# Performance work log

Hardware: AMD Instinct MI355X
Metric: run time of the kernel (lower is better)

Reference implementation:

```python
import jax, jax.numpy as jnp
import numpy as np

B, S, H = 2, 2048, 2048
NUM_HEADS, HEAD_DIM, GROUP_SIZE = 16, 128, 4
NUM_KV_HEADS = NUM_HEADS // GROUP_SIZE
ROPE_THETA = 10000.0


def setup_inputs() -> dict:
    key = jax.random.key(0)
    ks = jax.random.split(key, 10)
    xavier = lambda k, fi, fo: jax.random.uniform(k, (fi, fo), jnp.float32,
                                                  -jnp.sqrt(6.0 / (fi + fo)), jnp.sqrt(6.0 / (fi + fo)))
    hidden_states = jax.random.normal(ks[0], (B, S, H), jnp.float32)
    # causal mask: 1.0 where attention is disallowed (strictly upper triangle)
    mask = jnp.triu(jnp.ones((S, S), jnp.float32), k=1)[None, None, :, :]
    mask = jnp.broadcast_to(mask, (B, 1, S, S))
    return {
        "hidden_states": hidden_states,
        "mask": mask,
        "Wq": xavier(ks[1], H, NUM_HEADS * HEAD_DIM), "bq": jnp.zeros((NUM_HEADS * HEAD_DIM,), jnp.float32),
        "Wk": xavier(ks[2], H, NUM_KV_HEADS * HEAD_DIM), "bk": jnp.zeros((NUM_KV_HEADS * HEAD_DIM,), jnp.float32),
        "Wv": xavier(ks[3], H, NUM_KV_HEADS * HEAD_DIM), "bv": jnp.zeros((NUM_KV_HEADS * HEAD_DIM,), jnp.float32),
        "Wo": xavier(ks[4], NUM_HEADS * HEAD_DIM, H), "bo": jnp.zeros((H,), jnp.float32),
    }


def _apply_rope(q, k):
    # q: [b, s, hq, d], k: [b, s, hk, d]
    s, d = q.shape[1], q.shape[-1]
    inv_freq = 1.0 / (ROPE_THETA ** (jnp.arange(0, d, 2, dtype=jnp.float32) / d))  # [d/2]
    angles = jnp.arange(s, dtype=jnp.float32)[:, None] * inv_freq[None, :]          # [s, d/2]
    cos = jnp.cos(angles)[None, :, None, :]  # [1, s, 1, d/2]
    sin = jnp.sin(angles)[None, :, None, :]

    def rot(x):
        x1, x2 = jnp.split(x, 2, axis=-1)
        return jnp.concatenate([x1 * cos - x2 * sin, x1 * sin + x2 * cos], axis=-1)

    return rot(q), rot(k)


def reference(hidden_states, mask, Wq, bq, Wk, bk, Wv, bv, Wo, bo):
    b, s, _ = hidden_states.shape
    scale = 1.0 / jnp.sqrt(jnp.float32(HEAD_DIM))

    q = (hidden_states @ Wq + bq).reshape(b, s, NUM_HEADS, HEAD_DIM)
    k = (hidden_states @ Wk + bk).reshape(b, s, NUM_KV_HEADS, HEAD_DIM)
    v = (hidden_states @ Wv + bv).reshape(b, s, NUM_KV_HEADS, HEAD_DIM)

    q, k = _apply_rope(q, k)

    q = jnp.transpose(q, (0, 2, 1, 3))  # [b, hq, s, d]
    k = jnp.transpose(k, (0, 2, 1, 3))  # [b, hk, s, d]
    v = jnp.transpose(v, (0, 2, 1, 3))

    new_past_key, new_past_value = k, v

    # GQA: repeat each KV head group_size times
    k_rep = jnp.repeat(k, GROUP_SIZE, axis=1)  # [b, hq, s, d]
    v_rep = jnp.repeat(v, GROUP_SIZE, axis=1)

    attn_scores = jnp.einsum('bhqd,bhkd->bhqk', q, k_rep) * scale  # [b, hq, s, s]
    attn_scores = attn_scores + mask * -1e9
    attn_probs = jax.nn.softmax(attn_scores, axis=-1)
    attn_output = jnp.einsum('bhqk,bhkd->bhqd', attn_probs, v_rep)

    attn_output = attn_output.transpose(0, 2, 1, 3).reshape(b, s, NUM_HEADS * HEAD_DIM)
    attn_output = attn_output @ Wo + bo
    return attn_output, new_past_key, new_past_value
```

## Files before the change

### kernel.cpp

```cpp
#include <hip/hip_runtime.h>
#include <stdint.h>

#define S_LEN 2048
#define HDIM  2048
#define N_HEADS 16
#define HEAD_D 128
#define N_KV 4

typedef unsigned short u16;
typedef __attribute__((ext_vector_type(8))) short bf16x8;
typedef __attribute__((ext_vector_type(4))) short bf16x4;
typedef __attribute__((ext_vector_type(4))) float f32x4;

#define MFMA_PV(a, b, c) __builtin_amdgcn_mfma_f32_16x16x16bf16_1k(a, b, c, 0, 0, 0)

__device__ __forceinline__ u16 f2bf(float f) {
  unsigned u = __float_as_uint(f);
  u += 0x7FFFu + ((u >> 16) & 1u);
  return (u16)(u >> 16);
}

__device__ __forceinline__ float bf2f(u16 v) {
  return __uint_as_float(((unsigned)v) << 16);
}

__device__ __forceinline__ void gll16(void* lds, const void* gp) {
  __builtin_amdgcn_global_load_lds(
      (const __attribute__((address_space(1))) void*)gp,
      (__attribute__((address_space(3))) void*)lds, 16, 0, 0);
}

__device__ __forceinline__ void wtrans_body(
    const float* __restrict__ W, u16* __restrict__ Wt, int K, int N,
    int perm, int flat, float (*tile)[65]) {
  int k0 = (flat & 31) * 64, n0 = (flat >> 5) * 64;
  int tr = threadIdx.x >> 6, tc = threadIdx.x & 63;
#pragma unroll
  for (int i = 0; i < 16; ++i) {
    int r = tr + i * 4;
    tile[r][tc] = W[(size_t)(k0 + r) * N + n0 + tc];
  }
  __syncthreads();
#pragma unroll
  for (int i = 0; i < 16; ++i) {
    int r = tr + i * 4;
    int nn = n0 + r;
    if (perm)
      nn = (nn & ~127) | ((nn & 15) | ((nn & 48) << 1) | ((nn & 64) >> 2));
    Wt[(size_t)nn * K + k0 + tc] = f2bf(tile[tc][r]);
  }
}

__global__ __launch_bounds__(256) void k_prep(
    const float* __restrict__ hs, u16* __restrict__ Xbf,
    const float* __restrict__ Wq, u16* __restrict__ Wqt,
    const float* __restrict__ Wk, u16* __restrict__ Wkt,
    const float* __restrict__ Wv, u16* __restrict__ Wvt,
    const float* __restrict__ Wo, u16* __restrict__ Wot,
    float2* __restrict__ trig) {
  __shared__ float tile[64][65];
  const int bid = blockIdx.x;
  if (bid < 8192) {
    int i = bid * 256 + threadIdx.x;
    float4 v = ((const float4*)hs)[i];
    ushort4 o;
    o.x = f2bf(v.x); o.y = f2bf(v.y); o.z = f2bf(v.z); o.w = f2bf(v.w);
    ((ushort4*)Xbf)[i] = o;
  } else if (bid < 9216) {
    wtrans_body(Wq, Wqt, 2048, 2048, 1, bid - 8192, tile);
  } else if (bid < 9472) {
    wtrans_body(Wk, Wkt, 2048, 512, 1, bid - 9216, tile);
  } else if (bid < 9728) {
    wtrans_body(Wv, Wvt, 2048, 512, 0, bid - 9472, tile);
  } else if (bid < 10752) {
    wtrans_body(Wo, Wot, 2048, 2048, 0, bid - 9728, tile);
  } else {
    const float c1 = -13.287712379549449f / 64.f;
    int idx = (bid - 10752) * 256 + threadIdx.x;
    int s = idx >> 6, d1 = idx & 63;
    float fr = exp2f((float)d1 * c1);
    float sn, cs;
    sincosf((float)s * fr, &sn, &cs);
    trig[idx] = make_float2(cs, sn);
  }
}

__device__ __forceinline__ void gemm_main_128(
    const u16* __restrict__ A, const u16* __restrict__ Bt,
    int m0, int n0, int K, f32x4 (&acc)[4][4]) {
  __shared__ __align__(16) u16 sA[128 * 32];
  __shared__ __align__(16) u16 sB[128 * 32];
  const int tid = threadIdx.x;
  const int lane = tid & 63;
  const int wave = tid >> 6;
  const int quad = lane >> 4;
  const int l15 = lane & 15;
  const int wm = (wave >> 1) << 6;
  const int wn = (wave & 1) << 6;

#pragma unroll
  for (int i = 0; i < 4; ++i)
#pragma unroll
    for (int j = 0; j < 4; ++j)
      acc[i][j] = (f32x4){0.f, 0.f, 0.f, 0.f};

  for (int kk = 0; kk < K; kk += 32) {
    __syncthreads();
#pragma unroll
    for (int it = 0; it < 2; ++it) {
      int c = tid + (it << 8);
      int row = c >> 2;
      int ko = (c & 3) << 3;
      gll16((char*)sA + c * 16, A + (size_t)(m0 + row) * K + kk + ko);
      gll16((char*)sB + c * 16, Bt + (size_t)(n0 + row) * K + kk + ko);
    }
    __syncthreads();
    bf16x8 af[4], bfr[4];
#pragma unroll
    for (int i = 0; i < 4; ++i)
      af[i] = *(const bf16x8*)&sA[(wm + (i << 4) + l15) * 32 + quad * 8];
#pragma unroll
    for (int j = 0; j < 4; ++j)
      bfr[j] = *(const bf16x8*)&sB[(wn + (j << 4) + l15) * 32 + quad * 8];
#pragma unroll
    for (int i = 0; i < 4; ++i)
#pragma unroll
      for (int j = 0; j < 4; ++j)
        acc[i][j] = __builtin_amdgcn_mfma_f32_16x16x32_bf16(af[i], bfr[j], acc[i][j], 0, 0, 0);
  }
}

__device__ __forceinline__ void gemm_tile_128(
    const u16* __restrict__ A, const u16* __restrict__ Bt,
    const float* __restrict__ bias, float* __restrict__ C,
    int m0, int n0, int K, int ldc) {
  const int tid = threadIdx.x;
  const int lane = tid & 63;
  const int wave = tid >> 6;
  const int quad = lane >> 4;
  const int l15 = lane & 15;
  const int wm = (wave >> 1) << 6;
  const int wn = (wave & 1) << 6;

  f32x4 acc[4][4];
  gemm_main_128(A, Bt, m0, n0, K, acc);

#pragma unroll
  for (int i = 0; i < 4; ++i) {
    int row = m0 + wm + (i << 4) + quad * 4;
#pragma unroll
    for (int j = 0; j < 4; ++j) {
      int col = n0 + wn + (j << 4) + l15;
      float bv = bias[col];
      float* cp = C + (size_t)row * ldc + col;
#pragma unroll
      for (int r = 0; r < 4; ++r)
        cp[(size_t)r * ldc] = acc[i][j][r] + bv;
    }
  }
}

__global__ __launch_bounds__(256) void k_gemm_qkv_fused(
    const u16* __restrict__ X, const u16* __restrict__ Wqt,
    const u16* __restrict__ Wkt, const u16* __restrict__ Wvt,
    const float* __restrict__ bq, const float* __restrict__ bk,
    const float* __restrict__ bv, u16* __restrict__ Qbf,
    u16* __restrict__ Kbf, float* __restrict__ outK,
    u16* __restrict__ Vt, float* __restrict__ outV,
    const float2* __restrict__ trig) {
  const int m0 = blockIdx.x << 7;
  const int by = blockIdx.y;
  const int tid = threadIdx.x;
  const int lane = tid & 63;
  const int wave = tid >> 6;
  const int quad = lane >> 4;
  const int l15 = lane & 15;
  const int wm = (wave >> 1) << 6;
  const int wn = (wave & 1) << 6;

  const u16* Bt; int n0;
  if (by < 16)      { Bt = Wqt; n0 = by << 7; }
  else if (by < 20) { Bt = Wkt; n0 = (by - 16) << 7; }
  else              { Bt = Wvt; n0 = (by - 20) << 7; }

  f32x4 acc[4][4];
  gemm_main_128(X, Bt, m0, n0, 2048, acc);

  if (by < 16) {
    const float qscale = 0.08838834764831845f * 1.4426950408889634f;
    const int h = by;
#pragma unroll
    for (int jp = 0; jp < 2; ++jp) {
      const int d1 = (((wn >> 5) + jp) << 4) + l15;
      const float b1 = bq[h * 128 + d1];
      const float b2 = bq[h * 128 + d1 + 64];
#pragma unroll
      for (int i = 0; i < 4; ++i) {
        const int rowb = m0 + wm + (i << 4) + quad * 4;
#pragma unroll
        for (int r = 0; r < 4; ++r) {
          const int tok = rowb + r;
          const int b = tok >> 11, s = tok & 2047;
          const float2 t = trig[(s << 6) + d1];
          float x1 = acc[i][2 * jp][r] + b1;
          float x2 = acc[i][2 * jp + 1][r] + b2;
          u16* dst = Qbf + ((size_t)(b * N_HEADS + h) * S_LEN + s) * HEAD_D + d1;
          dst[0]  = f2bf((x1 * t.x - x2 * t.y) * qscale);
          dst[64] = f2bf((x1 * t.y + x2 * t.x) * qscale);
        }
      }
    }
  } else if (by < 20) {
    const int kvh = by - 16;
#pragma unroll
    for (int jp = 0; jp < 2; ++jp) {
      const int d1 = (((wn >> 5) + jp) << 4) + l15;
      const float b1 = bk[kvh * 128 + d1];
      const float b2 = bk[kvh * 128 + d1 + 64];
#pragma unroll
      for (int i = 0; i < 4; ++i) {
        const int rowb = m0 + wm + (i << 4) + quad * 4;
#pragma unroll
        for (int r = 0; r < 4; ++r) {
          const int tok = rowb + r;
          const int b = tok >> 11, s = tok & 2047;
          const float2 t = trig[(s << 6) + d1];
          float x1 = acc[i][2 * jp][r] + b1;
          float x2 = acc[i][2 * jp + 1][r] + b2;
          float o1 = x1 * t.x - x2 * t.y;
          float o2 = x1 * t.y + x2 * t.x;
          size_t idx = ((size_t)(b * N_KV + kvh) * S_LEN + s) * HEAD_D + d1;
          Kbf[idx]      = f2bf(o1);
          Kbf[idx + 64] = f2bf(o2);
          outK[idx]      = o1;
          outK[idx + 64] = o2;
        }
      }
    }
  } else {
    const int kvh = by - 20;
#pragma unroll
    for (int i = 0; i < 4; ++i) {
      const int rowb = m0 + wm + (i << 4) + quad * 4;
      const int b = rowb >> 11, s = rowb & 2047;
      const int z = b * N_KV + kvh;
#pragma unroll
      for (int j = 0; j < 4; ++j) {
        const int d = wn + (j << 4) + l15;
        const float bvv = bv[kvh * 128 + d];
        float v0 = acc[i][j][0] + bvv;
        float v1 = acc[i][j][1] + bvv;
        float v2 = acc[i][j][2] + bvv;
        float v3 = acc[i][j][3] + bvv;
        float* ov = outV + ((size_t)z * S_LEN + s) * HEAD_D + d;
        ov[0]   = v0;
        ov[128] = v1;
        ov[256] = v2;
        ov[384] = v3;
        ushort4 pk;
        pk.x = f2bf(v0); pk.y = f2bf(v1); pk.z = f2bf(v2); pk.w = f2bf(v3);
        *(ushort4*)(Vt + ((size_t)z * HEAD_D + d) * S_LEN + s) = pk;
      }
    }
  }
}

__global__ __launch_bounds__(256) void k_gemm_o(
    const u16* __restrict__ A, const u16* __restrict__ Wot,
    const float* __restrict__ bo, float* __restrict__ C) {
  gemm_tile_128(A, Wot, bo, C, blockIdx.x << 7, blockIdx.y << 7, 2048, 2048);
}

__global__ __launch_bounds__(256, 2) void k_attn(
    const u16* __restrict__ Qbf, const u16* __restrict__ Kbf,
    const u16* __restrict__ Vt, u16* __restrict__ attn,
    u16* __restrict__ pO, float* __restrict__ pML) {
  __shared__ __align__(16) u16 smem[17920];
  u16* sK = smem;
  u16* sV = smem + 8704;

  const int tid = threadIdx.x;
  const int lane = tid & 63;
  const int wave = tid >> 6;
  const int quad = lane >> 4;
  const int l15 = lane & 15;

  const int by = blockIdx.y;
  int qt, t0, t1, slot;
  bool finalw;
  if (by < 8) {
    qt = 8 + by; t0 = 0; t1 = 16; finalw = false;
    slot = ((blockIdx.x << 3) + (qt - 8)) << 1;
  } else {
    qt = 23 - by;
    if (qt >= 8) {
      t0 = 16; t1 = 2 * qt + 2; finalw = false;
      slot = (((blockIdx.x << 3) + (qt - 8)) << 1) + 1;
    } else {
      t0 = 0; t1 = 2 * qt + 2; finalw = true; slot = 0;
    }
  }

  const int bh = blockIdx.x;
  const int b = bh >> 4;
  const int h = bh & 15;
  const int kvh = h >> 2;
  const int q0 = qt << 7;
  const int qw = q0 + wave * 32;

  const u16* Qb = Qbf + ((size_t)(b * N_HEADS + h) * S_LEN + qw) * HEAD_D;
  const u16* Kb = Kbf + (size_t)(b * N_KV + kvh) * S_LEN * HEAD_D;
  const u16* Vb = Vt + (size_t)(b * N_KV + kvh) * HEAD_D * S_LEN;

  bf16x8 aq[2][4];
#pragma unroll
  for (int i = 0; i < 2; ++i)
#pragma unroll
    for (int kc = 0; kc < 4; ++kc)
      aq[i][kc] = *(const bf16x8*)(Qb + (size_t)(i * 16 + l15) * HEAD_D + kc * 32 + quad * 8);

  float mst[2] = {-1e30f, -1e30f}, lst[2] = {0.f, 0.f};
  f32x4 oacc[2][8];
#pragma unroll
  for (int i = 0; i < 2; ++i)
#pragma unroll
    for (int n = 0; n < 8; ++n) oacc[i][n] = (f32x4){0.f, 0.f, 0.f, 0.f};

  for (int t = t0; t < t1; ++t) {
    const int kt0 = t << 6;
    __syncthreads();
#pragma unroll
    for (int it = 0; it < 9; ++it) {
      int c = tid + (it << 8);
      if (c < 1088) {
        int row = c / 17;
        int k16 = c - row * 17;
        gll16((char*)sK + c * 16, Kb + (size_t)(kt0 + row) * HEAD_D + k16 * 8);
      } else if (c < 2240) {
        int vv = c - 1088;
        int d = vv / 9;
        int s16 = vv - d * 9;
        gll16((char*)sV + vv * 16, Vb + (size_t)d * S_LEN + kt0 + s16 * 8);
      }
    }
    __syncthreads();

    if (kt0 > qw + 31) continue;

    f32x4 st[2][4];
#pragma unroll
    for (int i = 0; i < 2; ++i)
#pragma unroll
      for (int j = 0; j < 4; ++j) st[i][j] = (f32x4){0.f, 0.f, 0.f, 0.f};
#pragma unroll
    for (int kc = 0; kc < 4; ++kc) {
#pragma unroll
      for (int j = 0; j < 4; ++j) {
        bf16x8 kf = *(const bf16x8*)&sK[(j * 16 + l15) * 136 + kc * 32 + quad * 8];
#pragma unroll
        for (int i = 0; i < 2; ++i)
          st[i][j] = __builtin_amdgcn_mfma_f32_16x16x32_bf16(kf, aq[i][kc], st[i][j], 0, 0, 0);
      }
    }

    if (kt0 + 63 > qw) {
#pragma unroll
      for (int i = 0; i < 2; ++i) {
        int q = qw + i * 16 + l15;
#pragma unroll
        for (int j = 0; j < 4; ++j) {
          int s = kt0 + j * 16 + quad * 4;
#pragma unroll
          for (int r = 0; r < 4; ++r)
            if (s + r > q) st[i][j][r] = -1e9f;
        }
      }
    }

    bf16x4 pf[2][4];
    float al[2];
#pragma unroll
    for (int i = 0; i < 2; ++i) {
      float m = -1e30f;
#pragma unroll
      for (int j = 0; j < 4; ++j)
#pragma unroll
        for (int r = 0; r < 4; ++r) m = fmaxf(m, st[i][j][r]);
      m = fmaxf(m, __shfl_xor(m, 16, 64));
      m = fmaxf(m, __shfl_xor(m, 32, 64));
      float mn = fmaxf(mst[i], m);
      al[i] = exp2f(mst[i] - mn);
      mst[i] = mn;
      float rs = 0.f;
#pragma unroll
      for (int j = 0; j < 4; ++j) {
        float p0 = exp2f(st[i][j][0] - mn);
        float p1 = exp2f(st[i][j][1] - mn);
        float p2 = exp2f(st[i][j][2] - mn);
        float p3 = exp2f(st[i][j][3] - mn);
        rs += (p0 + p1) + (p2 + p3);
        union { unsigned u[2]; bf16x4 v; } pk;
        pk.u[0] = __builtin_amdgcn_perm(__float_as_uint(p1) + 0x8000u,
                                        __float_as_uint(p0) + 0x8000u, 0x07060302u);
        pk.u[1] = __builtin_amdgcn_perm(__float_as_uint(p3) + 0x8000u,
                                        __float_as_uint(p2) + 0x8000u, 0x07060302u);
        pf[i][j] = pk.v;
      }
      rs += __shfl_xor(rs, 16, 64);
      rs += __shfl_xor(rs, 32, 64);
      lst[i] = lst[i] * al[i] + rs;
#pragma unroll
      for (int r = 0; r < 4; ++r) {
        float a = __shfl(al[i], quad * 4 + r, 16);
#pragma unroll
        for (int n = 0; n < 8; ++n) oacc[i][n][r] *= a;
      }
    }

#pragma unroll
    for (int j = 0; j < 4; ++j) {
#pragma unroll
      for (int n = 0; n < 8; ++n) {
        bf16x4 vf = *(const bf16x4*)&sV[(n * 16 + l15) * 72 + j * 16 + quad * 4];
#pragma unroll
        for (int i = 0; i < 2; ++i)
          oacc[i][n] = MFMA_PV(pf[i][j], vf, oacc[i][n]);
      }
    }
  }

  if (finalw) {
#pragma unroll
    for (int i = 0; i < 2; ++i)
#pragma unroll
      for (int r = 0; r < 4; ++r) {
        float inv = 1.0f / __shfl(lst[i], quad * 4 + r, 16);
        int row = qw + i * 16 + quad * 4 + r;
        u16* op = attn + ((size_t)b * S_LEN + row) * HDIM + h * HEAD_D;
#pragma unroll
        for (int n = 0; n < 8; ++n)
          op[n * 16 + l15] = f2bf(oacc[i][n][r] * inv);
      }
  } else {
    u16* po = pO + (size_t)slot * 16384;
#pragma unroll
    for (int i = 0; i < 2; ++i)
#pragma unroll
      for (int r = 0; r < 4; ++r) {
        int row = wave * 32 + i * 16 + quad * 4 + r;
#pragma unroll
        for (int n = 0; n < 8; ++n)
          po[row * 128 + n * 16 + l15] = f2bf(oacc[i][n][r]);
      }
    if (quad == 0) {
      float* ml = pML + slot * 256;
#pragma unroll
      for (int i = 0; i < 2; ++i) {
        int row = wave * 32 + i * 16 + l15;
        ml[row] = mst[i];
        ml[128 + row] = lst[i];
      }
    }
  }
}

__global__ __launch_bounds__(256) void k_attn_combine(
    const u16* __restrict__ pO, const float* __restrict__ pML,
    u16* __restrict__ attn) {
  const int bh = blockIdx.x;
  const int qt = 8 + blockIdx.y;
  const int b = bh >> 4;
  const int h = bh & 15;
  const int s0 = ((bh << 3) + blockIdx.y) << 1;
  const int row = threadIdx.x >> 1;
  const int half = threadIdx.x & 1;

  const float* ml0 = pML + s0 * 256;
  const float* ml1 = pML + (s0 + 1) * 256;
  float m0 = ml0[row], l0 = ml0[128 + row];
  float m1 = ml1[row], l1 = ml1[128 + row];
  float m = fmaxf(m0, m1);
  float w0 = exp2f(m0 - m), w1 = exp2f(m1 - m);
  float inv = 1.0f / (l0 * w0 + l1 * w1);
  w0 *= inv; w1 *= inv;

  const u16* o0 = pO + (size_t)s0 * 16384 + row * 128 + half * 64;
  const u16* o1 = o0 + 16384;
  u16* op = attn + ((size_t)(b * S_LEN + (qt << 7) + row)) * HDIM + h * HEAD_D + half * 64;
#pragma unroll
  for (int k = 0; k < 8; ++k) {
    ushort4 a0 = ((const ushort4*)o0)[k * 2];
    ushort4 b0 = ((const ushort4*)o0)[k * 2 + 1];
    ushort4 a1 = ((const ushort4*)o1)[k * 2];
    ushort4 b1 = ((const ushort4*)o1)[k * 2 + 1];
    ushort4 ra, rb;
    ra.x = f2bf(bf2f(a0.x) * w0 + bf2f(a1.x) * w1);
    ra.y = f2bf(bf2f(a0.y) * w0 + bf2f(a1.y) * w1);
    ra.z = f2bf(bf2f(a0.z) * w0 + bf2f(a1.z) * w1);
    ra.w = f2bf(bf2f(a0.w) * w0 + bf2f(a1.w) * w1);
    rb.x = f2bf(bf2f(b0.x) * w0 + bf2f(b1.x) * w1);
    rb.y = f2bf(bf2f(b0.y) * w0 + bf2f(b1.y) * w1);
    rb.z = f2bf(bf2f(b0.z) * w0 + bf2f(b1.z) * w1);
    rb.w = f2bf(bf2f(b0.w) * w0 + bf2f(b1.w) * w1);
    ((ushort4*)op)[k * 2] = ra;
    ((ushort4*)op)[k * 2 + 1] = rb;
  }
}

extern "C" void kernel_launch(void* const* d_in, const int* in_sizes, int n_in,
                              void* d_out, int out_size, void* d_ws, size_t ws_size,
                              hipStream_t stream) {
  (void)in_sizes; (void)n_in; (void)out_size; (void)ws_size;
  const float* hs = (const float*)d_in[0];
  const float* Wq = (const float*)d_in[2];
  const float* bq = (const float*)d_in[3];
  const float* Wk = (const float*)d_in[4];
  const float* bk = (const float*)d_in[5];
  const float* Wv = (const float*)d_in[6];
  const float* bv = (const float*)d_in[7];
  const float* Wo = (const float*)d_in[8];
  const float* bo = (const float*)d_in[9];
  float* out = (float*)d_out;

  char* ws = (char*)d_ws;
  u16* Xbf   = (u16*)(ws + 0);
  u16* Wqt   = (u16*)(ws + 16777216);
  u16* Wkt   = (u16*)(ws + 25165824);
  u16* Wvt   = (u16*)(ws + 27262976);
  u16* Wot   = (u16*)(ws + 29360128);
  u16* Qbf   = (u16*)(ws + 88080384);
  u16* Kbf   = (u16*)(ws + 104857600);
  u16* Vtb   = (u16*)(ws + 109051904);
  u16* attnb = (u16*)(ws + 37748736);
  float* pML = (float*)(ws + 54525952);
  float2* trg = (float2*)(ws + 56623104);
  u16* pO    = (u16*)(ws + 71303168);

  k_prep<<<11264, 256, 0, stream>>>(hs, Xbf, Wq, Wqt, Wk, Wkt, Wv, Wvt, Wo, Wot, trg);
  k_gemm_qkv_fused<<<dim3(32, 24), 256, 0, stream>>>(
      Xbf, Wqt, Wkt, Wvt, bq, bk, bv, Qbf, Kbf, out + 8388608,
      Vtb, out + 10485760, trg);
  k_attn<<<dim3(32, 24), 256, 0, stream>>>(Qbf, Kbf, Vtb, attnb, pO, pML);
  k_attn_combine<<<dim3(32, 8), 256, 0, stream>>>(pO, pML, attnb);
  k_gemm_o<<<dim3(32, 16), 256, 0, stream>>>(attnb, Wot, bo, out);
}
```

Baseline: 365.4 us.

## Rewrite fused QKV GEMM with 256x256 tiles and a ping-pong scheduled pipeline

The fused QKV projection now uses 512-thread blocks computing 256x256 tiles (grid 16x12), where it used 128x128 tiles. A double-buffered LDS pipeline with swizzled direct global-to-LDS loads, explicit barriers, waitcnts, setprio phases and 16x16x32 bf16 MFMAs overlaps loads with compute. The larger tiles raise data reuse and cut global traffic. The cost is a grid of only 192 blocks on a 256-CU part, so some CUs sit idle, plus heavy register pressure from the 8x4 accumulators. The RoPE and bias epilogue is remapped so that each wave covers half of one head.

```diff
diff --git a/kernel.cpp b/kernel.cpp
--- a/kernel.cpp
+++ b/kernel.cpp
@@ -160,7 +160,13 @@
   }
 }
 
-__global__ __launch_bounds__(256) void k_gemm_qkv_fused(
+__global__ __launch_bounds__(256) void k_gemm_o(
+    const u16* __restrict__ A, const u16* __restrict__ Wot,
+    const float* __restrict__ bo, float* __restrict__ C) {
+  gemm_tile_128(A, Wot, bo, C, blockIdx.x << 7, blockIdx.y << 7, 2048, 2048);
+}
+
+__global__ __launch_bounds__(512, 1) void k_gemm_qkv_fused(
     const u16* __restrict__ X, const u16* __restrict__ Wqt,
     const u16* __restrict__ Wkt, const u16* __restrict__ Wvt,
     const float* __restrict__ bq, const float* __restrict__ bk,
@@ -168,35 +174,134 @@
     u16* __restrict__ Kbf, float* __restrict__ outK,
     u16* __restrict__ Vt, float* __restrict__ outV,
     const float2* __restrict__ trig) {
-  const int m0 = blockIdx.x << 7;
-  const int by = blockIdx.y;
+  __shared__ __align__(16) u16 smem[32768];
   const int tid = threadIdx.x;
   const int lane = tid & 63;
   const int wave = tid >> 6;
   const int quad = lane >> 4;
   const int l15 = lane & 15;
-  const int wm = (wave >> 1) << 6;
-  const int wn = (wave & 1) << 6;
-
-  const u16* Bt; int n0;
-  if (by < 16)      { Bt = Wqt; n0 = by << 7; }
-  else if (by < 20) { Bt = Wkt; n0 = (by - 16) << 7; }
-  else              { Bt = Wvt; n0 = (by - 20) << 7; }
-
-  f32x4 acc[4][4];
-  gemm_main_128(X, Bt, m0, n0, 2048, acc);
-
-  if (by < 16) {
+  const int wmi = wave >> 2;
+  const int wn = wave & 3;
+  const int m0 = blockIdx.x << 8;
+  const int by = blockIdx.y;
+  (void)lane;
+
+  const u16* Btp; int n0l;
+  if (by < 8)       { Btp = Wqt; n0l = by << 8; }
+  else if (by < 10) { Btp = Wkt; n0l = (by - 8) << 8; }
+  else              { Btp = Wvt; n0l = (by - 10) << 8; }
+  const u16* Xp = X;
+
+  f32x4 acc[8][4];
+#pragma unroll
+  for (int i = 0; i < 8; ++i)
+#pragma unroll
+    for (int j = 0; j < 4; ++j) acc[i][j] = (f32x4){0.f, 0.f, 0.f, 0.f};
+  bf16x8 aR[4], bR[4];
+
+#define LDA_(b, row, k)                                                      \
+  (*(const bf16x8*)&smem[(b) * 16384 + (row) * 32 + ((k) ^ ((((row) >> 3) & 1) << 4))])
+#define LDB_(b, row, k)                                                      \
+  (*(const bf16x8*)&smem[(b) * 16384 + 8192 + (row) * 32 + ((k) ^ ((((row) >> 3) & 1) << 4))])
+
+#define STGA(t, h)                                                           \
+  {                                                                          \
+    int c_ = tid, cl_ = c_ ^ (((c_ >> 5) & 1) << 1);                         \
+    gll16((char*)smem + ((t) & 1) * 32768 + (h) * 8192 + c_ * 16,            \
+          Xp + (size_t)(m0 + (h) * 128 + (cl_ >> 2)) * 2048 + (t) * 32 + (cl_ & 3) * 8); \
+  }
+#define STGB(t, h)                                                           \
+  {                                                                          \
+    int c_ = tid, cl_ = c_ ^ (((c_ >> 5) & 1) << 1);                         \
+    gll16((char*)smem + ((t) & 1) * 32768 + 16384 + (h) * 8192 + c_ * 16,    \
+          Btp + (size_t)(n0l + (h) * 128 + (cl_ >> 2)) * 2048 + (t) * 32 + (cl_ & 3) * 8); \
+  }
+
+#define RDA(b, ih)                                                           \
+  _Pragma("unroll") for (int i_ = 0; i_ < 4; ++i_)                           \
+      aR[i_] = LDA_(b, wmi * 128 + (ih) * 64 + i_ * 16 + l15, quad * 8);
+#define RDB(b, jh)                                                           \
+  _Pragma("unroll") for (int j_ = 0; j_ < 2; ++j_)                           \
+      bR[(jh) * 2 + j_] = LDB_(b, wn * 64 + ((jh) * 2 + j_) * 16 + l15, quad * 8);
+#define MM(ih, jh)                                                           \
+  _Pragma("unroll") for (int i_ = 0; i_ < 4; ++i_)                           \
+  _Pragma("unroll") for (int j_ = 0; j_ < 2; ++j_)                           \
+      acc[(ih) * 4 + i_][(jh) * 2 + j_] = __builtin_amdgcn_mfma_f32_16x16x32_bf16( \
+          aR[i_], bR[(jh) * 2 + j_], acc[(ih) * 4 + i_][(jh) * 2 + j_], 0, 0, 0);
+
+#define PH_MID                                                               \
+  __builtin_amdgcn_s_barrier();                                              \
+  asm volatile("s_waitcnt lgkmcnt(0)" ::: "memory");                         \
+  __builtin_amdgcn_sched_barrier(0);                                         \
+  __builtin_amdgcn_s_setprio(1)
+#define PH_END                                                               \
+  __builtin_amdgcn_s_setprio(0);                                             \
+  __builtin_amdgcn_s_barrier()
+
+  STGA(0, 0); STGA(0, 1); STGB(0, 0); STGB(0, 1);
+  STGB(1, 0); STGB(1, 1);
+  asm volatile("s_waitcnt vmcnt(2)" ::: "memory");
+  __builtin_amdgcn_s_barrier();
+
+  for (int it = 0; it < 31; ++it) {
+    const int t1 = 2 * it + 1, tn0 = 2 * it + 2, tn1 = 2 * it + 3;
+    RDA(0, 0); RDB(0, 0); STGA(t1, 0); STGA(t1, 1);
+    PH_MID; MM(0, 0); PH_END;
+    RDB(0, 1);
+    PH_MID; MM(0, 1); PH_END;
+    RDA(0, 1); STGB(tn0, 0);
+    PH_MID; MM(1, 1); PH_END;
+    STGB(tn0, 1);
+    asm volatile("s_waitcnt vmcnt(2)" ::: "memory");
+    PH_MID; MM(1, 0); PH_END;
+    RDA(1, 0); RDB(1, 0); STGA(tn0, 0); STGA(tn0, 1);
+    PH_MID; MM(0, 0); PH_END;
+    RDB(1, 1);
+    PH_MID; MM(0, 1); PH_END;
+    RDA(1, 1); STGB(tn1, 0);
+    PH_MID; MM(1, 1); PH_END;
+    STGB(tn1, 1);
+    asm volatile("s_waitcnt vmcnt(2)" ::: "memory");
+    PH_MID; MM(1, 0); PH_END;
+  }
+  {
+    RDA(0, 0); RDB(0, 0); STGA(63, 0); STGA(63, 1);
+    PH_MID; MM(0, 0); PH_END;
+    RDB(0, 1);
+    PH_MID; MM(0, 1); PH_END;
+    RDA(0, 1);
+    PH_MID; MM(1, 1); PH_END;
+    asm volatile("s_waitcnt vmcnt(0)" ::: "memory");
+    PH_MID; MM(1, 0); PH_END;
+    RDA(1, 0); RDB(1, 0);
+    PH_MID; MM(0, 0); PH_END;
+    RDB(1, 1);
+    PH_MID; MM(0, 1); PH_END;
+    RDA(1, 1);
+    PH_MID; MM(1, 1); PH_END;
+    PH_MID; MM(1, 0); PH_END;
+  }
+#undef LDA_
+#undef LDB_
+#undef STGA
+#undef STGB
+#undef RDA
+#undef RDB
+#undef MM
+#undef PH_MID
+#undef PH_END
+
+  if (by < 8) {
     const float qscale = 0.08838834764831845f * 1.4426950408889634f;
-    const int h = by;
+    const int h = 2 * by + (wn >> 1);
 #pragma unroll
     for (int jp = 0; jp < 2; ++jp) {
-      const int d1 = (((wn >> 5) + jp) << 4) + l15;
+      const int d1 = l15 + (((wn & 1) * 2 + jp) << 4);
       const float b1 = bq[h * 128 + d1];
       const float b2 = bq[h * 128 + d1 + 64];
 #pragma unroll
-      for (int i = 0; i < 4; ++i) {
-        const int rowb = m0 + wm + (i << 4) + quad * 4;
+      for (int i = 0; i < 8; ++i) {
+        const int rowb = m0 + wmi * 128 + i * 16 + quad * 4;
 #pragma unroll
         for (int r = 0; r < 4; ++r) {
           const int tok = rowb + r;
@@ -210,16 +315,16 @@
         }
       }
     }
-  } else if (by < 20) {
-    const int kvh = by - 16;
+  } else if (by < 10) {
+    const int kvh = 2 * (by - 8) + (wn >> 1);
 #pragma unroll
     for (int jp = 0; jp < 2; ++jp) {
-      const int d1 = (((wn >> 5) + jp) << 4) + l15;
+      const int d1 = l15 + (((wn & 1) * 2 + jp) << 4);
       const float b1 = bk[kvh * 128 + d1];
       const float b2 = bk[kvh * 128 + d1 + 64];
 #pragma unroll
-      for (int i = 0; i < 4; ++i) {
-        const int rowb = m0 + wm + (i << 4) + quad * 4;
+      for (int i = 0; i < 8; ++i) {
+        const int rowb = m0 + wmi * 128 + i * 16 + quad * 4;
 #pragma unroll
         for (int r = 0; r < 4; ++r) {
           const int tok = rowb + r;
@@ -238,15 +343,15 @@
       }
     }
   } else {
-    const int kvh = by - 20;
-#pragma unroll
-    for (int i = 0; i < 4; ++i) {
-      const int rowb = m0 + wm + (i << 4) + quad * 4;
+    const int kvh = 2 * (by - 10) + (wn >> 1);
+#pragma unroll
+    for (int i = 0; i < 8; ++i) {
+      const int rowb = m0 + wmi * 128 + i * 16 + quad * 4;
       const int b = rowb >> 11, s = rowb & 2047;
       const int z = b * N_KV + kvh;
 #pragma unroll
       for (int j = 0; j < 4; ++j) {
-        const int d = wn + (j << 4) + l15;
+        const int d = (wn & 1) * 64 + j * 16 + l15;
         const float bvv = bv[kvh * 128 + d];
         float v0 = acc[i][j][0] + bvv;
         float v1 = acc[i][j][1] + bvv;
@@ -263,12 +368,6 @@
       }
     }
   }
-}
-
-__global__ __launch_bounds__(256) void k_gemm_o(
-    const u16* __restrict__ A, const u16* __restrict__ Wot,
-    const float* __restrict__ bo, float* __restrict__ C) {
-  gemm_tile_128(A, Wot, bo, C, blockIdx.x << 7, blockIdx.y << 7, 2048, 2048);
 }
 
 __global__ __launch_bounds__(256, 2) void k_attn(
@@ -537,7 +636,7 @@
   u16* pO    = (u16*)(ws + 71303168);
 
   k_prep<<<11264, 256, 0, stream>>>(hs, Xbf, Wq, Wqt, Wk, Wkt, Wv, Wvt, Wo, Wot, trg);
-  k_gemm_qkv_fused<<<dim3(32, 24), 256, 0, stream>>>(
+  k_gemm_qkv_fused<<<dim3(16, 12), 512, 0, stream>>>(
       Xbf, Wqt, Wkt, Wvt, bq, bk, bv, Qbf, Kbf, out + 8388608,
       Vtb, out + 10485760, trg);
   k_attn<<<dim3(32, 24), 256, 0, stream>>>(Qbf, Kbf, Vtb, attnb, pO, pML);
```

Result: faster. 344.5 us (-5.7%).
